# Kernel tuning notes

Hardware: AMD Instinct MI355X
Metric: run time of the kernel (lower is better)

Reference implementation:

```python
import jax, jax.numpy as jnp
import numpy as np

B, S, H = 2, 2048, 2048
NH, NKV, HD = 16, 4, 128
ROPE_BASE = 10000.0


def rotate_half(x):
    x1, x2 = jnp.split(x, 2, axis=-1)
    return jnp.concatenate((-x2, x1), axis=-1)


def setup_inputs() -> dict:
    key = jax.random.key(0)
    ks = jax.random.split(key, 6)
    hidden_states = jax.random.normal(ks[0], (B, S, H), dtype=jnp.float32)
    # additive causal mask, as used by HF: 0 on allowed, large negative on masked
    causal = jnp.triu(jnp.full((S, S), -1e9, dtype=jnp.float32), k=1)
    attention_mask = jnp.broadcast_to(causal[None, None], (B, 1, S, S))
    position_ids = jnp.broadcast_to(jnp.arange(S, dtype=jnp.int64)[None], (B, S))
    scale = 1.0 / np.sqrt(H)
    Wq = jax.random.normal(ks[1], (NH * HD, H), dtype=jnp.float32) * scale
    Wk = jax.random.normal(ks[2], (NKV * HD, H), dtype=jnp.float32) * scale
    Wv = jax.random.normal(ks[3], (NKV * HD, H), dtype=jnp.float32) * scale
    Wo = jax.random.normal(ks[4], (H, NH * HD), dtype=jnp.float32) * scale
    return {"hidden_states": hidden_states, "attention_mask": attention_mask,
            "position_ids": position_ids, "Wq": Wq, "Wk": Wk, "Wv": Wv, "Wo": Wo}


def reference(hidden_states, attention_mask, position_ids, Wq, Wk, Wv, Wo):
    b, s, _ = hidden_states.shape
    # projections (torch Linear: y = x W^T)
    q = jnp.einsum('bsh,oh->bso', hidden_states, Wq).reshape(b, s, NH, HD).transpose(0, 2, 1, 3)
    k = jnp.einsum('bsh,oh->bso', hidden_states, Wk).reshape(b, s, NKV, HD).transpose(0, 2, 1, 3)
    v = jnp.einsum('bsh,oh->bso', hidden_states, Wv).reshape(b, s, NKV, HD).transpose(0, 2, 1, 3)
    # RoPE
    inv_freq = 1.0 / (ROPE_BASE ** (jnp.arange(0, HD, 2, dtype=jnp.float32) / HD))  # [HD/2]
    freqs = position_ids.astype(jnp.float32)[:, :, None] * inv_freq[None, None, :]  # [B,S,HD/2]
    emb = jnp.concatenate((freqs, freqs), axis=-1)                                  # [B,S,HD]
    cos = jnp.cos(emb)[:, None]  # [B,1,S,HD]
    sin = jnp.sin(emb)[:, None]
    q = q * cos + rotate_half(q) * sin
    k = k * cos + rotate_half(k) * sin
    # GQA repeat (repeat_interleave along head axis)
    n_rep = NH // NKV
    k = jnp.repeat(k, n_rep, axis=1)
    v = jnp.repeat(v, n_rep, axis=1)
    scale = HD ** -0.5
    attn = jnp.einsum('bhqd,bhkd->bhqk', q, k) * scale
    attn = attn + attention_mask
    attn = jax.nn.softmax(attn.astype(jnp.float32), axis=-1).astype(q.dtype)
    out = jnp.einsum('bhqk,bhkd->bhqd', attn, v)            # [B,NH,S,HD]
    out = out.transpose(0, 2, 1, 3).reshape(b, s, NH * HD)  # [B,S,H]
    return jnp.einsum('bso,ho->bsh', out, Wo)
```

## Files before the change

### kernel.cpp

```cpp
#include <hip/hip_runtime.h>


#define B_ 2
#define S_ 2048
#define H_ 2048
#define NH_ 16
#define NKV_ 4
#define HD_ 128
#define QKV_N 3072

typedef unsigned short u16;
typedef unsigned int u32;
typedef unsigned long long u64;
typedef __attribute__((ext_vector_type(8))) short short8;
typedef __attribute__((ext_vector_type(4))) float floatx4;
typedef __attribute__((ext_vector_type(16))) float floatx16;

__device__ __forceinline__ u16 f2bf(float f) {
    union { float f; u32 u; } v; v.f = f;
    u32 u = v.u;
    return (u16)((u + 0x7fffu + ((u >> 16) & 1u)) >> 16);
}
__device__ __forceinline__ float bf2f(u16 h) {
    union { u32 u; float f; } v; v.u = ((u32)h) << 16;
    return v.f;
}
__device__ __forceinline__ void store_out(u16* p, float v)  { *p = f2bf(v); }
__device__ __forceinline__ void store_out(float* p, float v) { *p = v; }

__device__ __forceinline__ void gload_lds16(const void* g, void* l) {
    __builtin_amdgcn_global_load_lds(
        (const __attribute__((address_space(1))) void*)g,
        (__attribute__((address_space(3))) void*)l, 16, 0, 0);
}

__device__ __forceinline__ u32 cvtpk(float lo, float hi) {
    u32 r;
    asm("v_cvt_pk_bf16_f32 %0, %1, %2" : "=v"(r) : "v"(lo), "v"(hi));
    return r;
}

__device__ __forceinline__ void pl32swap(u32& a, u32& b) {
#if __has_builtin(__builtin_amdgcn_permlane32_swap)
    typedef __attribute__((ext_vector_type(2))) int iv2;
    iv2 r = __builtin_amdgcn_permlane32_swap((int)a, (int)b, false, false);
    a = (u32)r[0];
    b = (u32)r[1];
#else
    asm volatile("v_permlane32_swap_b32 %0, %1" : "+v"(a), "+v"(b));
#endif
}

__global__ __launch_bounds__(256) void cast_all(const float* __restrict__ hs,
                                                const float* __restrict__ Wq,
                                                const float* __restrict__ Wk,
                                                const float* __restrict__ Wv,
                                                const float* __restrict__ Wo,
                                                u16* __restrict__ hs_b,
                                                u16* __restrict__ wqkv_b,
                                                u16* __restrict__ wo_b) {
    int q = blockIdx.x * 256 + threadIdx.x;
    const float* src;
    u16* dst;
    if (q < 2097152)      { src = hs; dst = hs_b; }
    else if (q < 3145728) { q -= 2097152; src = Wq; dst = wqkv_b; }
    else if (q < 3407872) { q -= 3145728; src = Wk; dst = wqkv_b + 2048 * 2048; }
    else if (q < 3670016) { q -= 3407872; src = Wv; dst = wqkv_b + 2560 * 2048; }
    else                  { q -= 3670016; src = Wo; dst = wo_b; }
    float4 f = ((const float4*)src)[q];
    u32 lo = ((u32)f2bf(f.y) << 16) | f2bf(f.x);
    u32 hi2 = ((u32)f2bf(f.w) << 16) | f2bf(f.z);
    *(u64*)(dst + (size_t)q * 4) = (u64)lo | ((u64)hi2 << 32);
}

template <typename OutT>
__global__ __launch_bounds__(256) void gemm128(const u16* __restrict__ A,
                                               const u16* __restrict__ Bm,
                                               OutT* __restrict__ C,
                                               int M, int N, int K) {
    __shared__ __align__(16) u16 As[2][128][32];
    __shared__ __align__(16) u16 Bs[2][128][32];
    const int tid  = threadIdx.x;
    const int wave = tid >> 6;
    const int lane = tid & 63;
    const int quad = lane >> 4;
    const int l16  = lane & 15;

    const int nbx = gridDim.x, nby = gridDim.y;
    const int total = nbx * nby;
    int n = (int)blockIdx.y * nbx + (int)blockIdx.x;
    if ((total & 7) == 0) {
        int cpx = total >> 3;
        n = (n & 7) * cpx + (n >> 3);
    }
    const int m0 = (n / nbx) * 128;
    const int n0 = (n % nbx) * 128;

    const int wm = (wave >> 1) * 64;
    const int wn = (wave & 1) * 64;
    const int srow = tid >> 2;
    const int scol = (tid & 3) * 8;

    floatx4 acc[4][4] = {};

    const u16* a0 = A  + (size_t)(m0 + srow) * K + scol;
    const u16* a1 = A  + (size_t)(m0 + 64 + srow) * K + scol;
    const u16* b0 = Bm + (size_t)(n0 + srow) * K + scol;
    const u16* b1 = Bm + (size_t)(n0 + 64 + srow) * K + scol;

#define STAGE(buf, k0)                                            \
    do {                                                          \
        gload_lds16(a0 + (k0), &As[buf][srow][scol]);             \
        gload_lds16(a1 + (k0), &As[buf][64 + srow][scol]);        \
        gload_lds16(b0 + (k0), &Bs[buf][srow][scol]);             \
        gload_lds16(b1 + (k0), &Bs[buf][64 + srow][scol]);        \
    } while (0)

#define COMPUTE(buf)                                                        \
    do {                                                                    \
        short8 af[4], bfv[4];                                               \
        for (int i = 0; i < 4; ++i) {                                       \
            af[i]  = *(const short8*)&As[buf][wm + i * 16 + l16][quad * 8]; \
            bfv[i] = *(const short8*)&Bs[buf][wn + i * 16 + l16][quad * 8]; \
        }                                                                   \
        for (int mi = 0; mi < 4; ++mi)                                      \
            for (int ni = 0; ni < 4; ++ni)                                  \
                acc[mi][ni] = __builtin_amdgcn_mfma_f32_16x16x32_bf16(      \
                    af[mi], bfv[ni], acc[mi][ni], 0, 0, 0);                 \
    } while (0)

    STAGE(0, 0);
    __syncthreads();
    for (int k0 = 0; k0 < K; k0 += 64) {
        STAGE(1, k0 + 32);
        COMPUTE(0);
        __syncthreads();
        if (k0 + 64 < K) STAGE(0, k0 + 64);
        COMPUTE(1);
        __syncthreads();
    }
#undef STAGE
#undef COMPUTE

    for (int mi = 0; mi < 4; ++mi)
        for (int ni = 0; ni < 4; ++ni)
            for (int r = 0; r < 4; ++r) {
                int row = m0 + wm + mi * 16 + quad * 4 + r;
                int col = n0 + wn + ni * 16 + l16;
                store_out(C + (size_t)row * N + col, acc[mi][ni][r]);
            }
}

__global__ __launch_bounds__(256) void gemm_bn64(const u16* __restrict__ A,
                                                 const u16* __restrict__ Bm,
                                                 float* __restrict__ C,
                                                 int M, int N, int K) {
    __shared__ __align__(16) u16 As[2][128][32];
    __shared__ __align__(16) u16 Bs[2][64][32];
    const int tid  = threadIdx.x;
    const int wave = tid >> 6;
    const int lane = tid & 63;
    const int quad = lane >> 4;
    const int l16  = lane & 15;

    const int nbx = gridDim.x, nby = gridDim.y;
    const int total = nbx * nby;
    int n = (int)blockIdx.y * nbx + (int)blockIdx.x;
    if ((total & 7) == 0) {
        int cpx = total >> 3;
        n = (n & 7) * cpx + (n >> 3);
    }
    const int m0 = (n / nbx) * 128;
    const int n0 = (n % nbx) * 64;

    const int wm = (wave >> 1) * 64;
    const int wn = (wave & 1) * 32;
    const int srow = tid >> 2;
    const int scol = (tid & 3) * 8;

    floatx4 acc[4][2] = {};

    const u16* a0 = A  + (size_t)(m0 + srow) * K + scol;
    const u16* a1 = A  + (size_t)(m0 + 64 + srow) * K + scol;
    const u16* b0 = Bm + (size_t)(n0 + srow) * K + scol;

#define STAGE(buf, k0)                                            \
    do {                                                          \
        gload_lds16(a0 + (k0), &As[buf][srow][scol]);             \
        gload_lds16(a1 + (k0), &As[buf][64 + srow][scol]);        \
        gload_lds16(b0 + (k0), &Bs[buf][srow][scol]);             \
    } while (0)

#define COMPUTE(buf)                                                        \
    do {                                                                    \
        short8 af[4], bfv[2];                                               \
        for (int i = 0; i < 4; ++i)                                         \
            af[i]  = *(const short8*)&As[buf][wm + i * 16 + l16][quad * 8]; \
        for (int i = 0; i < 2; ++i)                                         \
            bfv[i] = *(const short8*)&Bs[buf][wn + i * 16 + l16][quad * 8]; \
        for (int mi = 0; mi < 4; ++mi)                                      \
            for (int ni = 0; ni < 2; ++ni)                                  \
                acc[mi][ni] = __builtin_amdgcn_mfma_f32_16x16x32_bf16(      \
                    af[mi], bfv[ni], acc[mi][ni], 0, 0, 0);                 \
    } while (0)

    STAGE(0, 0);
    __syncthreads();
    for (int k0 = 0; k0 < K; k0 += 64) {
        STAGE(1, k0 + 32);
        COMPUTE(0);
        __syncthreads();
        if (k0 + 64 < K) STAGE(0, k0 + 64);
        COMPUTE(1);
        __syncthreads();
    }
#undef STAGE
#undef COMPUTE

    for (int mi = 0; mi < 4; ++mi)
        for (int ni = 0; ni < 2; ++ni)
            for (int r = 0; r < 4; ++r) {
                int row = m0 + wm + mi * 16 + quad * 4 + r;
                int col = n0 + wn + ni * 16 + l16;
                C[(size_t)row * N + col] = acc[mi][ni][r];
            }
}

__global__ __launch_bounds__(256) void rope_trans(u16* __restrict__ buf,
                                                  u16* __restrict__ vt) {
    const int bid = blockIdx.x;
    const int tid = threadIdx.x;
    if (bid < 20480) {
        int i = bid * 256 + tid;
        int hofs, nheads;
        float oscale;
        if (i < 4194304) { hofs = 0;    nheads = 16; oscale = 0.08838834764831845f; }
        else             { i -= 4194304; hofs = 2048; nheads = 4;  oscale = 1.0f; }
        int d = i & 63;
        int t = i >> 6;
        int head = t % nheads;
        int row  = t / nheads;
        int s    = row & (S_ - 1);
        size_t base = (size_t)row * QKV_N + hofs + head * HD_;
        float invf = exp2f(-(float)d * (13.28771237954945f / 64.0f));
        float fr = (float)s * invf;
        float sn, cs;
        sincosf(fr, &sn, &cs);
        float x1 = bf2f(buf[base + d]);
        float x2 = bf2f(buf[base + d + 64]);
        buf[base + d]      = f2bf((x1 * cs - x2 * sn) * oscale);
        buf[base + d + 64] = f2bf((x2 * cs + x1 * sn) * oscale);
    } else {
        __shared__ u16 t[32][33];
        const int b2 = bid - 20480;
        const int bx = b2 & 15, by = (b2 >> 4) & 63, bz = b2 >> 10;
        const int tx = tid & 31, ty = tid >> 5;
        const int c0 = bx * 32, s0 = by * 32, b = bz;
        for (int i = 0; i < 4; ++i)
            t[ty + i * 8][tx] =
                buf[((size_t)(b * S_ + s0 + ty + i * 8)) * QKV_N + 2560 + c0 + tx];
        __syncthreads();
        for (int i = 0; i < 4; ++i)
            vt[((size_t)(b * 512 + c0 + ty + i * 8)) * S_ + s0 + tx] = t[tx][ty + i * 8];
    }
}

__global__ __launch_bounds__(256) void flash_attn(const u16* __restrict__ qkv,
                                                  const u16* __restrict__ vtg,
                                                  u16* __restrict__ o) {
    __shared__ __align__(16) u16 KsL[64 * 128];
    __shared__ __align__(16) u16 VtL[128 * 64];

    const int tid  = threadIdx.x;
    const int wave = tid >> 6;
    const int lane = tid & 63;
    const int l31  = lane & 31;
    const int hi   = lane >> 5;
    const int wq   = wave >> 1;
    const int kb   = wave & 1;

    const int bx = (int)blockIdx.x;
    const int by = (int)blockIdx.y;
    const int b    = (bx >> 2) & 1;
    const int kvh  = bx & 3;
    const int h    = kvh * 4 + (by & 3);
    const int jqRaw = ((by >> 2) << 2) | (bx >> 3);
    const int quad = jqRaw >> 3;
    const int base = jqRaw & 7;
    int jq;
    if      (quad == 0) jq = 31 - base;
    else if (quad == 1) jq = 16 + base;
    else if (quad == 2) jq = 15 - base;
    else                jq = base;
    const int q0  = jq * 64;

    const size_t qb = ((size_t)(b * S_ + q0 + wq * 32 + l31)) * QKV_N + h * HD_;
    short8 qf[8];
#pragma unroll
    for (int mf = 0; mf < 8; ++mf)
        qf[mf] = *(const short8*)(qkv + qb + mf * 16 + hi * 8);

    floatx16 o_acc[4] = {};
    float l_loc = 0.f;

    const size_t kbase = (size_t)(b * S_) * QKV_N + 2048 + kvh * HD_;
    const size_t vbase = (size_t)((b * NKV_ + kvh) * HD_) * S_;
    const int krow_l = (lane >> 4);
    const int kslot  = lane & 15;
    const int vrow_l = (lane >> 3);
    const int vslot  = lane & 7;
    int kr_[4], kc_[4], vr_[4], vc_[4];
#pragma unroll
    for (int p = 0; p < 4; ++p) {
        kr_[p] = 16 * wave + 4 * p + krow_l;
        kc_[p] = (kslot ^ (kr_[p] & 7)) * 8;
        vr_[p] = 32 * wave + 8 * p + vrow_l;
        vc_[p] = (vslot ^ (vr_[p] & 7)) * 8;
    }

    const int rk = kb * 32 + l31;
    const int kswz = rk & 7;

    short8 kreg[4], vreg[4];
#pragma unroll
    for (int p = 0; p < 4; ++p) {
        kreg[p] = *(const short8*)(qkv + kbase + (size_t)kr_[p] * QKV_N + kc_[p]);
        vreg[p] = *(const short8*)(vtg + vbase + (size_t)vr_[p] * S_ + vc_[p]);
    }

    for (int kt = 0; kt <= jq; ++kt) {
        __syncthreads();
#pragma unroll
        for (int p = 0; p < 4; ++p) {
            *(short8*)&KsL[(16 * wave + 4 * p) * 128 + lane * 8] = kreg[p];
            *(short8*)&VtL[(32 * wave + 8 * p) * 64 + lane * 8]  = vreg[p];
        }
        __syncthreads();

        if (kt < jq) {
            const size_t ko = kbase + (size_t)((kt + 1) * 64) * QKV_N;
            const size_t vo = vbase + (size_t)((kt + 1) * 64);
#pragma unroll
            for (int p = 0; p < 4; ++p) {
                kreg[p] = *(const short8*)(qkv + ko + (size_t)kr_[p] * QKV_N + kc_[p]);
                vreg[p] = *(const short8*)(vtg + vo + (size_t)vr_[p] * S_ + vc_[p]);
            }
        }

        floatx16 st = {};
#pragma unroll
        for (int mf = 0; mf < 8; ++mf) {
            short8 kf = *(const short8*)&KsL[rk * 128 + (((mf * 2 + hi) ^ kswz) * 8)];
            st = __builtin_amdgcn_mfma_f32_32x32x16_bf16(kf, qf[mf], st, 0, 0, 0);
        }
        if (kt == jq) {
            int qloc = wq * 32 + l31;
#pragma unroll
            for (int r = 0; r < 16; ++r) {
                int krow = kb * 32 + (r & 3) + 8 * (r >> 2) + 4 * hi;
                if (krow > qloc) st[r] = -INFINITY;
            }
        }
        u32 pk[8];
        float ll = 0.f;
#pragma unroll
        for (int i = 0; i < 8; ++i) {
            float e0 = __expf(st[2 * i]);
            float e1 = __expf(st[2 * i + 1]);
            ll += e0 + e1;
            pk[i] = cvtpk(e0, e1);
        }
        l_loc += ll;
        pl32swap(pk[0], pk[2]);
        pl32swap(pk[1], pk[3]);
        pl32swap(pk[4], pk[6]);
        pl32swap(pk[5], pk[7]);
        union { u32 u[4]; short8 s; } c0, c1;
        c0.u[0] = pk[0]; c0.u[1] = pk[1]; c0.u[2] = pk[2]; c0.u[3] = pk[3];
        c1.u[0] = pk[4]; c1.u[1] = pk[5]; c1.u[2] = pk[6]; c1.u[3] = pk[7];
#pragma unroll
        for (int dblk = 0; dblk < 4; ++dblk) {
            int rv = dblk * 32 + l31;
            int sw = rv & 7;
            short8 va = *(const short8*)&VtL[rv * 64 + (((kb * 4 + hi) ^ sw) * 8)];
            o_acc[dblk] = __builtin_amdgcn_mfma_f32_32x32x16_bf16(va, c0.s, o_acc[dblk], 0, 0, 0);
            short8 vb = *(const short8*)&VtL[rv * 64 + (((kb * 4 + 2 + hi) ^ sw) * 8)];
            o_acc[dblk] = __builtin_amdgcn_mfma_f32_32x32x16_bf16(vb, c1.s, o_acc[dblk], 0, 0, 0);
        }
    }

    float lt = l_loc + __shfl_xor(l_loc, 32, 64);
    __syncthreads();
    float* scr = (float*)KsL;
    if (kb == 1) scr[wq * 64 + lane] = lt;
    __syncthreads();
    float linv = 0.f;
    if (kb == 0) linv = 1.0f / (lt + scr[wq * 64 + lane]);

#pragma unroll
    for (int dblk = 0; dblk < 4; ++dblk) {
        __syncthreads();
        if (kb == 1) {
#pragma unroll
            for (int r = 0; r < 16; ++r)
                scr[wq * 1088 + lane * 17 + r] = o_acc[dblk][r];
        }
        __syncthreads();
        if (kb == 0) {
            const int row = q0 + wq * 32 + l31;
#pragma unroll
            for (int rg = 0; rg < 4; ++rg) {
                float v0 = (o_acc[dblk][rg * 4 + 0] + scr[wq * 1088 + lane * 17 + rg * 4 + 0]) * linv;
                float v1 = (o_acc[dblk][rg * 4 + 1] + scr[wq * 1088 + lane * 17 + rg * 4 + 1]) * linv;
                float v2 = (o_acc[dblk][rg * 4 + 2] + scr[wq * 1088 + lane * 17 + rg * 4 + 2]) * linv;
                float v3 = (o_acc[dblk][rg * 4 + 3] + scr[wq * 1088 + lane * 17 + rg * 4 + 3]) * linv;
                u32 wlo = cvtpk(v0, v1);
                u32 whi = cvtpk(v2, v3);
                int col = h * HD_ + dblk * 32 + rg * 8 + 4 * hi;
                u64 pack = (u64)wlo | ((u64)whi << 32);
                *(u64*)(o + ((size_t)(b * S_ + row)) * H_ + col) = pack;
            }
        }
    }
}

extern "C" void kernel_launch(void* const* d_in, const int* in_sizes, int n_in,
                              void* d_out, int out_size, void* d_ws, size_t ws_size,
                              hipStream_t stream) {
    const float* hs = (const float*)d_in[0];
    const float* Wq = (const float*)d_in[3];
    const float* Wk = (const float*)d_in[4];
    const float* Wv = (const float*)d_in[5];
    const float* Wo = (const float*)d_in[6];

    char* ws = (char*)d_ws;
    const size_t MB = 1024 * 1024;
    u16* hs_b   = (u16*)(ws + 0);
    u16* wqkv_b = (u16*)(ws + 16 * MB);
    u16* vt_b   = (u16*)(ws + 16 * MB);
    u16* wo_b   = (u16*)(ws + 28 * MB);
    u16* qkv    = (u16*)(ws + 36 * MB);

    const int M = B_ * S_;

    cast_all<<<18432, 256, 0, stream>>>(hs, Wq, Wk, Wv, Wo, hs_b, wqkv_b, wo_b);

    gemm128<u16><<<dim3(QKV_N / 128, M / 128), 256, 0, stream>>>(
        hs_b, wqkv_b, qkv, M, QKV_N, H_);

    rope_trans<<<22528, 256, 0, stream>>>(qkv, vt_b);

    flash_attn<<<dim3(32, 32), 256, 0, stream>>>(qkv, vt_b, hs_b);

    gemm_bn64<<<dim3(H_ / 64, M / 128), 256, 0, stream>>>(
        hs_b, wo_b, (float*)d_out, M, H_, H_);
}
```

Baseline: 327.4 us.

## Fuse RoPE and V transpose into the QKV GEMM epilogue via swizzled LDS

Removes the separate rope_trans kernel. The QKV GEMM now writes its bf16 tile into a swizzled shared-memory buffer, then applies RoPE and scaling to the Q/K columns, or writes the V columns transposed straight to the vt buffer. This saves a full read/write pass over the QKV activations and one kernel launch. In exchange the GEMM gets a longer epilogue with sincos work and an extra barrier, and the vt buffer moves to its own workspace region because it can no longer alias the weights still being read.

```diff
diff --git a/kernel.cpp b/kernel.cpp
--- a/kernel.cpp
+++ b/kernel.cpp
@@ -25,8 +25,6 @@
     union { u32 u; float f; } v; v.u = ((u32)h) << 16;
     return v.f;
 }
-__device__ __forceinline__ void store_out(u16* p, float v)  { *p = f2bf(v); }
-__device__ __forceinline__ void store_out(float* p, float v) { *p = v; }
 
 __device__ __forceinline__ void gload_lds16(const void* g, void* l) {
     __builtin_amdgcn_global_load_lds(
@@ -73,13 +71,18 @@
     *(u64*)(dst + (size_t)q * 4) = (u64)lo | ((u64)hi2 << 32);
 }
 
-template <typename OutT>
-__global__ __launch_bounds__(256) void gemm128(const u16* __restrict__ A,
-                                               const u16* __restrict__ Bm,
-                                               OutT* __restrict__ C,
-                                               int M, int N, int K) {
-    __shared__ __align__(16) u16 As[2][128][32];
-    __shared__ __align__(16) u16 Bs[2][128][32];
+#define ASW(buf, r, c) SM[(buf) * 4096 + (r) * 32 + (c)]
+#define BSW(buf, r, c) SM[8192 + (buf) * 4096 + (r) * 32 + (c)]
+__device__ __forceinline__ int tix(int r, int c) {
+    return r * 128 + (c ^ ((r & 31) << 1));
+}
+
+__global__ __launch_bounds__(256) void gemm_qkv(const u16* __restrict__ A,
+                                                const u16* __restrict__ Bm,
+                                                u16* __restrict__ qkv,
+                                                u16* __restrict__ vt) {
+    __shared__ __align__(16) u16 SM[16384];
+    const int K = 2048;
     const int tid  = threadIdx.x;
     const int wave = tid >> 6;
     const int lane = tid & 63;
@@ -110,23 +113,23 @@
 
 #define STAGE(buf, k0)                                            \
     do {                                                          \
-        gload_lds16(a0 + (k0), &As[buf][srow][scol]);             \
-        gload_lds16(a1 + (k0), &As[buf][64 + srow][scol]);        \
-        gload_lds16(b0 + (k0), &Bs[buf][srow][scol]);             \
-        gload_lds16(b1 + (k0), &Bs[buf][64 + srow][scol]);        \
+        gload_lds16(a0 + (k0), &ASW(buf, srow, scol));            \
+        gload_lds16(a1 + (k0), &ASW(buf, 64 + srow, scol));       \
+        gload_lds16(b0 + (k0), &BSW(buf, srow, scol));            \
+        gload_lds16(b1 + (k0), &BSW(buf, 64 + srow, scol));       \
     } while (0)
 
-#define COMPUTE(buf)                                                        \
-    do {                                                                    \
-        short8 af[4], bfv[4];                                               \
-        for (int i = 0; i < 4; ++i) {                                       \
-            af[i]  = *(const short8*)&As[buf][wm + i * 16 + l16][quad * 8]; \
-            bfv[i] = *(const short8*)&Bs[buf][wn + i * 16 + l16][quad * 8]; \
-        }                                                                   \
-        for (int mi = 0; mi < 4; ++mi)                                      \
-            for (int ni = 0; ni < 4; ++ni)                                  \
-                acc[mi][ni] = __builtin_amdgcn_mfma_f32_16x16x32_bf16(      \
-                    af[mi], bfv[ni], acc[mi][ni], 0, 0, 0);                 \
+#define COMPUTE(buf)                                                         \
+    do {                                                                     \
+        short8 af[4], bfv[4];                                                \
+        for (int i = 0; i < 4; ++i) {                                        \
+            af[i]  = *(const short8*)&ASW(buf, wm + i * 16 + l16, quad * 8); \
+            bfv[i] = *(const short8*)&BSW(buf, wn + i * 16 + l16, quad * 8); \
+        }                                                                    \
+        for (int mi = 0; mi < 4; ++mi)                                       \
+            for (int ni = 0; ni < 4; ++ni)                                   \
+                acc[mi][ni] = __builtin_amdgcn_mfma_f32_16x16x32_bf16(       \
+                    af[mi], bfv[ni], acc[mi][ni], 0, 0, 0);                  \
     } while (0)
 
     STAGE(0, 0);
@@ -144,12 +147,45 @@
 
     for (int mi = 0; mi < 4; ++mi)
         for (int ni = 0; ni < 4; ++ni)
-            for (int r = 0; r < 4; ++r) {
-                int row = m0 + wm + mi * 16 + quad * 4 + r;
-                int col = n0 + wn + ni * 16 + l16;
-                store_out(C + (size_t)row * N + col, acc[mi][ni][r]);
-            }
-}
+            for (int r = 0; r < 4; ++r)
+                SM[tix(wm + mi * 16 + quad * 4 + r, wn + ni * 16 + l16)] =
+                    f2bf(acc[mi][ni][r]);
+    __syncthreads();
+
+    const int bb = m0 >> 11;
+    const int s0 = m0 & 2047;
+
+    if (n0 < 2560) {
+        const float osc = (n0 < 2048) ? 0.08838834764831845f : 1.0f;
+#pragma unroll 4
+        for (int it = 0; it < 32; ++it) {
+            int idx = it * 256 + tid;
+            int r = idx >> 6;
+            int d = idx & 63;
+            float x1 = bf2f(SM[tix(r, d)]);
+            float x2 = bf2f(SM[tix(r, d + 64)]);
+            int s = s0 + r;
+            float invf = exp2f(-(float)d * (13.28771237954945f / 64.0f));
+            float fr = (float)s * invf;
+            float sn, cs;
+            sincosf(fr, &sn, &cs);
+            size_t base = (size_t)(m0 + r) * QKV_N + n0 + d;
+            qkv[base]      = f2bf((x1 * cs - x2 * sn) * osc);
+            qkv[base + 64] = f2bf((x2 * cs + x1 * sn) * osc);
+        }
+    } else {
+        const int cg0 = n0 - 2560;
+#pragma unroll 4
+        for (int it = 0; it < 64; ++it) {
+            int idx = it * 256 + tid;
+            int c = idx >> 7;
+            int s = idx & 127;
+            vt[((size_t)(bb * 512 + cg0 + c)) * S_ + s0 + s] = SM[tix(s, c)];
+        }
+    }
+}
+#undef ASW
+#undef BSW
 
 __global__ __launch_bounds__(256) void gemm_bn64(const u16* __restrict__ A,
                                                  const u16* __restrict__ Bm,
@@ -224,45 +260,6 @@
                 int col = n0 + wn + ni * 16 + l16;
                 C[(size_t)row * N + col] = acc[mi][ni][r];
             }
-}
-
-__global__ __launch_bounds__(256) void rope_trans(u16* __restrict__ buf,
-                                                  u16* __restrict__ vt) {
-    const int bid = blockIdx.x;
-    const int tid = threadIdx.x;
-    if (bid < 20480) {
-        int i = bid * 256 + tid;
-        int hofs, nheads;
-        float oscale;
-        if (i < 4194304) { hofs = 0;    nheads = 16; oscale = 0.08838834764831845f; }
-        else             { i -= 4194304; hofs = 2048; nheads = 4;  oscale = 1.0f; }
-        int d = i & 63;
-        int t = i >> 6;
-        int head = t % nheads;
-        int row  = t / nheads;
-        int s    = row & (S_ - 1);
-        size_t base = (size_t)row * QKV_N + hofs + head * HD_;
-        float invf = exp2f(-(float)d * (13.28771237954945f / 64.0f));
-        float fr = (float)s * invf;
-        float sn, cs;
-        sincosf(fr, &sn, &cs);
-        float x1 = bf2f(buf[base + d]);
-        float x2 = bf2f(buf[base + d + 64]);
-        buf[base + d]      = f2bf((x1 * cs - x2 * sn) * oscale);
-        buf[base + d + 64] = f2bf((x2 * cs + x1 * sn) * oscale);
-    } else {
-        __shared__ u16 t[32][33];
-        const int b2 = bid - 20480;
-        const int bx = b2 & 15, by = (b2 >> 4) & 63, bz = b2 >> 10;
-        const int tx = tid & 31, ty = tid >> 5;
-        const int c0 = bx * 32, s0 = by * 32, b = bz;
-        for (int i = 0; i < 4; ++i)
-            t[ty + i * 8][tx] =
-                buf[((size_t)(b * S_ + s0 + ty + i * 8)) * QKV_N + 2560 + c0 + tx];
-        __syncthreads();
-        for (int i = 0; i < 4; ++i)
-            vt[((size_t)(b * 512 + c0 + ty + i * 8)) * S_ + s0 + tx] = t[tx][ty + i * 8];
-    }
 }
 
 __global__ __launch_bounds__(256) void flash_attn(const u16* __restrict__ qkv,
@@ -437,18 +434,16 @@
     const size_t MB = 1024 * 1024;
     u16* hs_b   = (u16*)(ws + 0);
     u16* wqkv_b = (u16*)(ws + 16 * MB);
-    u16* vt_b   = (u16*)(ws + 16 * MB);
     u16* wo_b   = (u16*)(ws + 28 * MB);
     u16* qkv    = (u16*)(ws + 36 * MB);
+    u16* vt_b   = (u16*)(ws + 60 * MB);
 
     const int M = B_ * S_;
 
     cast_all<<<18432, 256, 0, stream>>>(hs, Wq, Wk, Wv, Wo, hs_b, wqkv_b, wo_b);
 
-    gemm128<u16><<<dim3(QKV_N / 128, M / 128), 256, 0, stream>>>(
-        hs_b, wqkv_b, qkv, M, QKV_N, H_);
-
-    rope_trans<<<22528, 256, 0, stream>>>(qkv, vt_b);
+    gemm_qkv<<<dim3(QKV_N / 128, M / 128), 256, 0, stream>>>(
+        hs_b, wqkv_b, qkv, vt_b);
 
     flash_attn<<<dim3(32, 32), 256, 0, stream>>>(qkv, vt_b, hs_b);
 
```

Measured after the change: 323.3 us. Within noise of the previous version (-1.2%).
